# Performance work log

Measured on AMD Instinct MI355X. Metric: run time of the kernel, lower is better.

The kernel has to match this reference:

```python
import jax, jax.numpy as jnp
import numpy as np

N = 100000      # nodes
E = 1600000     # edges
G = 512         # graphs in batch
C_IN = 128
H = 256
C_OUT = 10
L = 4           # num_layers
BN_EPS = 1e-5


def setup_inputs() -> dict:
    key = jax.random.key(0)
    ks = jax.random.split(key, 24)
    x = jax.random.normal(ks[0], (N, C_IN), dtype=jnp.float32)
    src = jax.random.randint(ks[1], (E,), 0, N, dtype=jnp.int32)
    dst = jax.random.randint(ks[2], (E,), 0, N, dtype=jnp.int32)
    batch = jnp.sort(jax.random.randint(ks[3], (N,), 0, G, dtype=jnp.int32))
    s_in = 1.0 / np.sqrt(C_IN)
    s_h = 1.0 / np.sqrt(H)
    # layer 0 GIN MLP (C_IN -> H -> H)
    W1_0 = jax.random.normal(ks[4], (C_IN, H), dtype=jnp.float32) * s_in
    b1_0 = jnp.zeros((H,), dtype=jnp.float32)
    W2_0 = jax.random.normal(ks[5], (H, H), dtype=jnp.float32) * s_h
    b2_0 = jnp.zeros((H,), dtype=jnp.float32)
    # layers 1..L-1 GIN MLPs (H -> H -> H), stacked
    W1_r = jax.random.normal(ks[6], (L - 1, H, H), dtype=jnp.float32) * s_h
    b1_r = jnp.zeros((L - 1, H), dtype=jnp.float32)
    W2_r = jax.random.normal(ks[7], (L - 1, H, H), dtype=jnp.float32) * s_h
    b2_r = jnp.zeros((L - 1, H), dtype=jnp.float32)
    # BatchNorm (inference / running stats) per layer
    bn_gamma = jnp.ones((L, H), dtype=jnp.float32)
    bn_beta = jnp.zeros((L, H), dtype=jnp.float32)
    bn_mean = jax.random.normal(ks[8], (L, H), dtype=jnp.float32) * 0.1
    bn_var = jax.random.uniform(ks[9], (L, H), dtype=jnp.float32, minval=0.5, maxval=1.5)
    Wc = jax.random.normal(ks[10], (H, C_OUT), dtype=jnp.float32) * s_h
    bc = jnp.zeros((C_OUT,), dtype=jnp.float32)
    return dict(x=x, src=src, dst=dst, batch=batch,
                W1_0=W1_0, b1_0=b1_0, W2_0=W2_0, b2_0=b2_0,
                W1_r=W1_r, b1_r=b1_r, W2_r=W2_r, b2_r=b2_r,
                bn_gamma=bn_gamma, bn_beta=bn_beta, bn_mean=bn_mean, bn_var=bn_var,
                Wc=Wc, bc=bc)


def _gin_layer(x, src, dst, W1, b1, W2, b2, gamma, beta, mean, var):
    # GIN aggregation (eps=0): (1+eps)*x + sum over incoming neighbors
    agg = jax.ops.segment_sum(x[src], dst, num_segments=N)  # gather-scatter over edges
    h = x + agg
    # 2-layer MLP
    h = jax.nn.relu(h @ W1 + b1) @ W2 + b2
    # BatchNorm1d (eval, running stats) + ReLU; dropout is identity in eval
    h = (h - mean) * (gamma * jax.lax.rsqrt(var + BN_EPS)) + beta
    return jax.nn.relu(h)


def reference(x, src, dst, batch, W1_0, b1_0, W2_0, b2_0,
              W1_r, b1_r, W2_r, b2_r, bn_gamma, bn_beta, bn_mean, bn_var, Wc, bc):
    h = _gin_layer(x, src, dst, W1_0, b1_0, W2_0, b2_0,
                   bn_gamma[0], bn_beta[0], bn_mean[0], bn_var[0])
    for i in range(L - 1):
        h = _gin_layer(h, src, dst, W1_r[i], b1_r[i], W2_r[i], b2_r[i],
                       bn_gamma[i + 1], bn_beta[i + 1], bn_mean[i + 1], bn_var[i + 1])
    # global_mean_pool over graphs
    sums = jax.ops.segment_sum(h, batch, num_segments=G)            # [G, H]
    cnt = jax.ops.segment_sum(jnp.ones((N,), h.dtype), batch, num_segments=G)
    pooled = sums / jnp.maximum(cnt, 1.0)[:, None]
    return pooled @ Wc + bc
```

## Files before the change

kernel.cpp:

```cpp
#include <hip/hip_runtime.h>
#include <stdint.h>

#define NN 100000
#define NE 1600000
#define NG 512
#define NB_SCAN ((NN + 1023) / 1024)
#define BSH 8
#define NBUK ((NN + 255) >> 8)
#define BCAP 5120
#define P1CH 4096
#define NP1 ((NE + P1CH - 1) / P1CH)

typedef __attribute__((ext_vector_type(2))) float f32x2;
typedef __attribute__((ext_vector_type(2))) unsigned short u16x2;
typedef __attribute__((ext_vector_type(4))) unsigned short u16x4;
typedef __attribute__((ext_vector_type(4))) unsigned int u32x4;
typedef __attribute__((ext_vector_type(4))) int i32x4;
typedef __attribute__((ext_vector_type(8))) short bf16x8;
typedef __attribute__((ext_vector_type(4))) float f32x4;
typedef unsigned long long u64;

__device__ __forceinline__ float bf2f(unsigned short u) {
  union { unsigned int i; float f; } v; v.i = ((unsigned int)u) << 16; return v.f;
}
__device__ __forceinline__ unsigned short f2bf(float f) {
  union { float f; unsigned int i; } v; v.f = f;
  unsigned int x = v.i;
  return (unsigned short)((x + 0x7fffu + ((x >> 16) & 1u)) >> 16);
}

__global__ __launch_bounds__(256) void p1_kernel(const int* __restrict__ src,
                                                 const int* __restrict__ dst,
                                                 int* __restrict__ bcur,
                                                 u64* __restrict__ pairs) {
  __shared__ u64 buf[P1CH];
  __shared__ int cnt[NBUK], off[NBUK], place[NBUK], gbase[NBUK];
  int tid = threadIdx.x;
  int e0 = blockIdx.x * P1CH;
  int ecnt = min(P1CH, NE - e0);
  for (int i = tid; i < NBUK; i += 256) cnt[i] = 0;
  __syncthreads();
  int ls[16], ld[16];
#pragma unroll
  for (int k = 0; k < 16; ++k) {
    int i = tid + k * 256;
    if (i < ecnt) {
      ls[k] = src[e0 + i];
      ld[k] = dst[e0 + i];
      atomicAdd(&cnt[ld[k] >> BSH], 1);
    }
  }
  __syncthreads();
  if (tid < 64) {
    int base = tid * 7;
    int loc[7];
    int s = 0;
#pragma unroll
    for (int k = 0; k < 7; ++k) {
      int idx = base + k;
      int v = (idx < NBUK) ? cnt[idx] : 0;
      loc[k] = s; s += v;
    }
    int incl = s;
    for (int o = 1; o < 64; o <<= 1) {
      int t = __shfl_up(incl, o, 64);
      if (tid >= o) incl += t;
    }
    int ex = incl - s;
#pragma unroll
    for (int k = 0; k < 7; ++k) {
      int idx = base + k;
      if (idx < NBUK) { off[idx] = ex + loc[k]; place[idx] = ex + loc[k]; }
    }
  }
  __syncthreads();
  for (int b = tid; b < NBUK; b += 256)
    if (cnt[b] > 0) gbase[b] = atomicAdd(&bcur[b], cnt[b]);
  __syncthreads();
#pragma unroll
  for (int k = 0; k < 16; ++k) {
    int i = tid + k * 256;
    if (i < ecnt) {
      int b = ld[k] >> BSH;
      int p = atomicAdd(&place[b], 1);
      buf[p] = ((u64)(unsigned)ld[k] << 32) | (unsigned)ls[k];
    }
  }
  __syncthreads();
  for (int i = tid; i < ecnt; i += 256) {
    u64 pr = buf[i];
    int b = (int)(pr >> 32) >> BSH;
    int idx = gbase[b] + (i - off[b]);
    pairs[(size_t)b * BCAP + idx] = pr;
  }
}

__global__ __launch_bounds__(256) void bcount_kernel(const u64* __restrict__ pairs,
                                                     const int* __restrict__ bcur,
                                                     int* __restrict__ ncnt) {
  int b = blockIdx.x, tid = threadIdx.x;
  __shared__ int cnt[256];
  cnt[tid] = 0;
  __syncthreads();
  int n = bcur[b];
  const u64* pp = pairs + (size_t)b * BCAP;
  for (int i = tid; i < n; i += 256) {
    int d = (int)(pp[i] >> 32);
    atomicAdd(&cnt[d & 255], 1);
  }
  __syncthreads();
  int node = (b << BSH) + tid;
  if (node < NN) ncnt[node] = cnt[tid];
}

__global__ __launch_bounds__(256) void p2_kernel(const u64* __restrict__ pairs,
                                                 const int* __restrict__ bcur,
                                                 const int* __restrict__ rowptr,
                                                 int* __restrict__ esrc) {
  int b = blockIdx.x, tid = threadIdx.x;
  __shared__ int cur[256];
  int node = (b << BSH) + tid;
  cur[tid] = (node < NN) ? rowptr[node] : 0;
  __syncthreads();
  int n = bcur[b];
  const u64* pp = pairs + (size_t)b * BCAP;
  for (int i = tid; i < n; i += 256) {
    u64 pr = pp[i];
    int s = (int)(pr & 0xffffffffu);
    int d = (int)(pr >> 32);
    int p = atomicAdd(&cur[d & 255], 1);
    esrc[p] = s;
  }
}

__global__ __launch_bounds__(256) void bsum_kernel(const int* __restrict__ counts,
                                                   int* __restrict__ bsums) {
  __shared__ int red[256];
  int b = blockIdx.x, tid = threadIdx.x;
  int s = 0;
#pragma unroll
  for (int k = 0; k < 4; ++k) {
    int i = b * 1024 + k * 256 + tid;
    if (i < NN) s += counts[i];
  }
  red[tid] = s;
  __syncthreads();
  for (int off = 128; off > 0; off >>= 1) {
    if (tid < off) red[tid] += red[tid + off];
    __syncthreads();
  }
  if (tid == 0) bsums[b] = red[0];
}

__global__ __launch_bounds__(128) void bscan_kernel(const int* __restrict__ bsums,
                                                    int* __restrict__ boff,
                                                    int* __restrict__ rowptr) {
  __shared__ int buf[128];
  int tid = threadIdx.x;
  int v = (tid < NB_SCAN) ? bsums[tid] : 0;
  buf[tid] = v;
  __syncthreads();
  int incl = v;
  for (int off = 1; off < 128; off <<= 1) {
    int add = (tid >= off) ? buf[tid - off] : 0;
    __syncthreads();
    incl += add;
    buf[tid] = incl;
    __syncthreads();
  }
  if (tid < NB_SCAN) boff[tid] = incl - v;
  if (tid == NB_SCAN - 1) rowptr[NN] = incl;
}

__global__ __launch_bounds__(256) void scan_apply_kernel(const int* __restrict__ counts,
                                                         const int* __restrict__ boff,
                                                         int* __restrict__ rowptr) {
  __shared__ int tsum[256];
  int b = blockIdx.x, tid = threadIdx.x;
  int base = b * 1024 + tid * 4;
  int c[4];
  if (base + 3 < NN) {
    i32x4 cv = *(const i32x4*)(counts + base);
    c[0] = cv[0]; c[1] = cv[1]; c[2] = cv[2]; c[3] = cv[3];
  } else {
#pragma unroll
    for (int k = 0; k < 4; ++k) c[k] = (base + k < NN) ? counts[base + k] : 0;
  }
  int s = c[0] + c[1] + c[2] + c[3];
  tsum[tid] = s;
  __syncthreads();
  int incl = s;
  for (int off = 1; off < 256; off <<= 1) {
    int add = (tid >= off) ? tsum[tid - off] : 0;
    __syncthreads();
    incl += add;
    tsum[tid] = incl;
    __syncthreads();
  }
  int ex = boff[b] + incl - s;
#pragma unroll
  for (int k = 0; k < 4; ++k) {
    int i = base + k;
    if (i < NN) rowptr[i] = ex;
    ex += c[k];
  }
}

__global__ __launch_bounds__(256) void convx_kernel(const float* __restrict__ x,
                                                    unsigned short* __restrict__ xb) {
  int t = blockIdx.x * 256 + threadIdx.x;
  int i = t * 4;
  if (i < NN * 128) {
    f32x4 v = *(const f32x4*)(x + i);
    u16x4 o;
    o[0] = f2bf(v[0]); o[1] = f2bf(v[1]); o[2] = f2bf(v[2]); o[3] = f2bf(v[3]);
    *(u16x4*)(xb + i) = o;
  }
}

__global__ __launch_bounds__(256) void wconv_kernel(const float* __restrict__ W,
                                                    unsigned short* __restrict__ Wt,
                                                    int K, int ncols) {
  int t = blockIdx.x * 256 + threadIdx.x;
  if (t < K * ncols) {
    int k = t / ncols, n = t % ncols;
    Wt[n * K + k] = f2bf(W[t]);
  }
}

__global__ __launch_bounds__(256) void bnprep_kernel(const float* __restrict__ gamma,
                                                     const float* __restrict__ beta,
                                                     const float* __restrict__ mean,
                                                     const float* __restrict__ var,
                                                     float* __restrict__ scale,
                                                     float* __restrict__ shift) {
  int t = blockIdx.x * 256 + threadIdx.x;
  if (t < 4 * 256) {
    float s = gamma[t] * rsqrtf(var[t] + 1e-5f);
    scale[t] = s;
    shift[t] = beta[t] - mean[t] * s;
  }
}

__device__ __forceinline__ void deq4(int w, float s, float& a0, float& a1, float& a2, float& a3) {
  a0 += s * (float)((w << 24) >> 24);
  a1 += s * (float)((w << 16) >> 24);
  a2 += s * (float)((w << 8) >> 24);
  a3 += s * (float)(w >> 24);
}

__global__ __launch_bounds__(256, 8) void agg256_kernel(const signed char* __restrict__ hq,
                                                        const float* __restrict__ hs,
                                                        const int* __restrict__ rowptr,
                                                        const int* __restrict__ esrc,
                                                        unsigned short* __restrict__ out) {
  int node = blockIdx.x * 4 + (threadIdx.x >> 6);
  int lane = threadIdx.x & 63;
  if (node >= NN) return;
  const int* __restrict__ hv = (const int*)hq;
  float a0 = 0.f, a1 = 0.f, a2 = 0.f, a3 = 0.f;
  deq4(hv[(size_t)node * 64 + lane], hs[node], a0, a1, a2, a3);
  int p = rowptr[node];
  const int pe = rowptr[node + 1];
  for (; p + 16 <= pe; p += 16) {
    int idx[16];
#pragma unroll
    for (int j = 0; j < 16; ++j) idx[j] = esrc[p + j];
    int w[16]; float sc[16];
#pragma unroll
    for (int j = 0; j < 16; ++j) { w[j] = hv[(size_t)idx[j] * 64 + lane]; sc[j] = hs[idx[j]]; }
#pragma unroll
    for (int j = 0; j < 16; ++j) deq4(w[j], sc[j], a0, a1, a2, a3);
  }
  for (; p + 4 <= pe; p += 4) {
    int idx[4];
#pragma unroll
    for (int j = 0; j < 4; ++j) idx[j] = esrc[p + j];
    int w[4]; float sc[4];
#pragma unroll
    for (int j = 0; j < 4; ++j) { w[j] = hv[(size_t)idx[j] * 64 + lane]; sc[j] = hs[idx[j]]; }
#pragma unroll
    for (int j = 0; j < 4; ++j) deq4(w[j], sc[j], a0, a1, a2, a3);
  }
  for (; p < pe; ++p) deq4(hv[(size_t)esrc[p] * 64 + lane], hs[esrc[p]], a0, a1, a2, a3);
  u16x4 o; o[0] = f2bf(a0); o[1] = f2bf(a1); o[2] = f2bf(a2); o[3] = f2bf(a3);
  union { u16x4 v; u64 q; } cv; cv.v = o;
  __builtin_nontemporal_store(cv.q, (u64*)out + (size_t)node * 64 + lane);
}

__global__ __launch_bounds__(256, 8) void agg128_kernel(const unsigned short* __restrict__ h,
                                                        const int* __restrict__ rowptr,
                                                        const int* __restrict__ esrc,
                                                        unsigned short* __restrict__ out) {
  int node = blockIdx.x * 4 + (threadIdx.x >> 6);
  int lane = threadIdx.x & 63;
  if (node >= NN) return;
  const u16x2* __restrict__ hv = (const u16x2*)h;
  u16x2 v = hv[(size_t)node * 64 + lane];
  float a0 = bf2f(v[0]), a1 = bf2f(v[1]);
  int p = rowptr[node];
  const int pe = rowptr[node + 1];
  for (; p + 8 <= pe; p += 8) {
    int idx[8];
#pragma unroll
    for (int j = 0; j < 8; ++j) idx[j] = esrc[p + j];
    u16x2 u[8];
#pragma unroll
    for (int j = 0; j < 8; ++j) u[j] = hv[(size_t)idx[j] * 64 + lane];
#pragma unroll
    for (int j = 0; j < 8; ++j) { a0 += bf2f(u[j][0]); a1 += bf2f(u[j][1]); }
  }
  for (; p < pe; ++p) {
    u16x2 u = hv[(size_t)esrc[p] * 64 + lane];
    a0 += bf2f(u[0]); a1 += bf2f(u[1]);
  }
  u16x2 o; o[0] = f2bf(a0); o[1] = f2bf(a1);
  ((u16x2*)out)[(size_t)node * 64 + lane] = o;
}

template <int K>
__global__ __launch_bounds__(256, 4) void mlp_kernel(
    const unsigned short* __restrict__ hin, const unsigned short* __restrict__ W1t,
    const float* __restrict__ b1, const unsigned short* __restrict__ W2t,
    const float* __restrict__ b2, const float* __restrict__ bnscale,
    const float* __restrict__ bnshift, signed char* __restrict__ hq,
    float* __restrict__ hscale, int M) {
  constexpr int AP = K + 8;
  constexpr int SP = 264;
  __shared__ unsigned short buf[64 * 264];
  __shared__ float wmax[4][64];
  __shared__ float rowinv[64];
  int tid = threadIdx.x;
  int lane = tid & 63, w = tid >> 6;
  int l16 = lane & 15, lhi = lane >> 4;
  int row0 = blockIdx.x * 64;

  constexpr int CH = 64 * K / 8;
  for (int ch = tid; ch < CH; ch += 256) {
    int r = ch / (K / 8);
    int c = (ch % (K / 8)) * 8;
    u32x4 val = {0u, 0u, 0u, 0u};
    if (row0 + r < M) val = *(const u32x4*)(hin + (size_t)(row0 + r) * K + c);
    *(u32x4*)(&buf[r * AP + c]) = val;
  }
  __syncthreads();

  f32x4 acc[4][4] = {};
#pragma unroll
  for (int ks = 0; ks < K / 32; ++ks) {
    int kk = ks * 32 + lhi * 8;
    bf16x8 a[4], b[4];
#pragma unroll
    for (int mf = 0; mf < 4; ++mf)
      a[mf] = *(const bf16x8*)(&buf[(16 * mf + l16) * AP + kk]);
#pragma unroll
    for (int nf = 0; nf < 4; ++nf)
      b[nf] = *(const bf16x8*)(W1t + (size_t)(64 * w + 16 * nf + l16) * K + kk);
#pragma unroll
    for (int mf = 0; mf < 4; ++mf)
#pragma unroll
      for (int nf = 0; nf < 4; ++nf)
        acc[mf][nf] = __builtin_amdgcn_mfma_f32_16x16x32_bf16(a[mf], b[nf], acc[mf][nf], 0, 0, 0);
  }
  __syncthreads();

#pragma unroll
  for (int nf = 0; nf < 4; ++nf) {
    int col = 64 * w + 16 * nf + l16;
    float bias = b1[col];
#pragma unroll
    for (int mf = 0; mf < 4; ++mf) {
      f32x4 v = acc[mf][nf];
#pragma unroll
      for (int j = 0; j < 4; ++j) {
        float x = v[j] + bias;
        x = fmaxf(x, 0.f);
        buf[(16 * mf + lhi * 4 + j) * SP + col] = f2bf(x);
      }
    }
  }
  __syncthreads();

  f32x4 acc2[4][4] = {};
#pragma unroll
  for (int ks = 0; ks < 8; ++ks) {
    int kk = ks * 32 + lhi * 8;
    bf16x8 a[4], b[4];
#pragma unroll
    for (int mf = 0; mf < 4; ++mf)
      a[mf] = *(const bf16x8*)(&buf[(16 * mf + l16) * SP + kk]);
#pragma unroll
    for (int nf = 0; nf < 4; ++nf)
      b[nf] = *(const bf16x8*)(W2t + (size_t)(64 * w + 16 * nf + l16) * 256 + kk);
#pragma unroll
    for (int mf = 0; mf < 4; ++mf)
#pragma unroll
      for (int nf = 0; nf < 4; ++nf)
        acc2[mf][nf] = __builtin_amdgcn_mfma_f32_16x16x32_bf16(a[mf], b[nf], acc2[mf][nf], 0, 0, 0);
  }

  float pmax[4][4];
#pragma unroll
  for (int mf = 0; mf < 4; ++mf)
#pragma unroll
    for (int j = 0; j < 4; ++j) pmax[mf][j] = 0.f;
#pragma unroll
  for (int nf = 0; nf < 4; ++nf) {
    int col = 64 * w + 16 * nf + l16;
    float bias = b2[col], sc = bnscale[col], sh = bnshift[col];
#pragma unroll
    for (int mf = 0; mf < 4; ++mf) {
#pragma unroll
      for (int j = 0; j < 4; ++j) {
        float x = acc2[mf][nf][j] + bias;
        x = x * sc + sh;
        x = fmaxf(x, 0.f);
        acc2[mf][nf][j] = x;
        pmax[mf][j] = fmaxf(pmax[mf][j], x);
      }
    }
  }
#pragma unroll
  for (int mf = 0; mf < 4; ++mf) {
#pragma unroll
    for (int j = 0; j < 4; ++j) {
      float m = pmax[mf][j];
      m = fmaxf(m, __shfl_xor(m, 1, 16));
      m = fmaxf(m, __shfl_xor(m, 2, 16));
      m = fmaxf(m, __shfl_xor(m, 4, 16));
      m = fmaxf(m, __shfl_xor(m, 8, 16));
      pmax[mf][j] = m;
    }
  }
  if (l16 == 0) {
#pragma unroll
    for (int mf = 0; mf < 4; ++mf)
#pragma unroll
      for (int j = 0; j < 4; ++j)
        wmax[w][16 * mf + lhi * 4 + j] = pmax[mf][j];
  }
  __syncthreads();
  if (tid < 64) {
    float m = fmaxf(fmaxf(wmax[0][tid], wmax[1][tid]), fmaxf(wmax[2][tid], wmax[3][tid]));
    m = fmaxf(m, 1e-20f);
    rowinv[tid] = 127.f / m;
    int r = row0 + tid;
    if (r < M) hscale[r] = m * (1.f / 127.f);
  }
  __syncthreads();
#pragma unroll
  for (int mf = 0; mf < 4; ++mf) {
#pragma unroll
    for (int j = 0; j < 4; ++j) {
      int lr = 16 * mf + lhi * 4 + j;
      int r = row0 + lr;
      if (r < M) {
        float inv = rowinv[lr];
#pragma unroll
        for (int nf = 0; nf < 4; ++nf) {
          int col = 64 * w + 16 * nf + l16;
          int q = __float2int_rn(acc2[mf][nf][j] * inv);
          hq[(size_t)r * 256 + col] = (signed char)q;
        }
      }
    }
  }
}

__global__ __launch_bounds__(256) void pool_classify_kernel(
    const signed char* __restrict__ hq, const float* __restrict__ hs,
    const int* __restrict__ batch, const float* __restrict__ Wc,
    const float* __restrict__ bc, float* __restrict__ out) {
  int g = blockIdx.x;
  int tid = threadIdx.x;
  __shared__ int bounds[2];
  if (tid < 2) {
    int target = g + tid;
    int lo = 0, hi = NN;
    while (lo < hi) {
      int mid = (lo + hi) >> 1;
      if (batch[mid] < target) lo = mid + 1; else hi = mid;
    }
    bounds[tid] = lo;
  }
  __syncthreads();
  int s = bounds[0], e = bounds[1];
  float sum = 0.f;
  for (int i = s; i < e; ++i)
    sum += hs[i] * (float)hq[(size_t)i * 256 + tid];
  int cnt = e - s;
  float p = sum / (float)(cnt > 1 ? cnt : 1);
  __shared__ float red[256];
  for (int c = 0; c < 10; ++c) {
    red[tid] = p * Wc[tid * 10 + c];
    __syncthreads();
    for (int off = 128; off > 0; off >>= 1) {
      if (tid < off) red[tid] += red[tid + off];
      __syncthreads();
    }
    if (tid == 0) out[g * 10 + c] = red[0] + bc[c];
    __syncthreads();
  }
}

extern "C" void kernel_launch(void* const* d_in, const int* in_sizes, int n_in,
                              void* d_out, int out_size, void* d_ws, size_t ws_size,
                              hipStream_t stream) {
  const float* x = (const float*)d_in[0];
  const int* src = (const int*)d_in[1];
  const int* dst = (const int*)d_in[2];
  const int* batch = (const int*)d_in[3];
  const float* W1_0 = (const float*)d_in[4];
  const float* b1_0 = (const float*)d_in[5];
  const float* W2_0 = (const float*)d_in[6];
  const float* b2_0 = (const float*)d_in[7];
  const float* W1_r = (const float*)d_in[8];
  const float* b1_r = (const float*)d_in[9];
  const float* W2_r = (const float*)d_in[10];
  const float* b2_r = (const float*)d_in[11];
  const float* bn_gamma = (const float*)d_in[12];
  const float* bn_beta = (const float*)d_in[13];
  const float* bn_mean = (const float*)d_in[14];
  const float* bn_var = (const float*)d_in[15];
  const float* Wc = (const float*)d_in[16];
  const float* bc = (const float*)d_in[17];
  float* out = (float*)d_out;

  char* base = (char*)d_ws;
  size_t off = 0;
  auto take = [&](size_t bytes) {
    size_t cur = off;
    off += (bytes + 255) & ~(size_t)255;
    return cur;
  };
  int* bcur = (int*)(base + take((size_t)NBUK * 4));
  u64* pairs = (u64*)(base + take((size_t)NBUK * BCAP * 8));
  int* ncnt = (int*)(base + take((size_t)NN * 4));
  int* rowptr = (int*)(base + take((size_t)(NN + 1) * 4));
  int* esrc = (int*)(base + take((size_t)NE * 4));
  unsigned short* xb = (unsigned short*)(base + take((size_t)NN * 128 * 2));
  signed char* hq = (signed char*)(base + take((size_t)NN * 256));
  float* hscale = (float*)(base + take((size_t)NN * 4));
  unsigned short* hin = (unsigned short*)(base + take((size_t)NN * 256 * 2));
  unsigned short* W1_0t = (unsigned short*)(base + take(256 * 128 * 2));
  unsigned short* W2_0t = (unsigned short*)(base + take(256 * 256 * 2));
  unsigned short* W1_rt = (unsigned short*)(base + take(3 * 256 * 256 * 2));
  unsigned short* W2_rt = (unsigned short*)(base + take(3 * 256 * 256 * 2));
  float* bnscale = (float*)(base + take(4 * 256 * 4));
  float* bnshift = (float*)(base + take(4 * 256 * 4));
  int* bsums = (int*)(base + take(NB_SCAN * 4));
  int* boff = (int*)(base + take(NB_SCAN * 4));
  (void)ws_size; (void)in_sizes; (void)n_in; (void)out_size;

  (void)hipMemsetAsync(bcur, 0, (size_t)NBUK * 4, stream);
  p1_kernel<<<NP1, 256, 0, stream>>>(src, dst, bcur, pairs);
  bcount_kernel<<<NBUK, 256, 0, stream>>>(pairs, bcur, ncnt);
  bsum_kernel<<<NB_SCAN, 256, 0, stream>>>(ncnt, bsums);
  bscan_kernel<<<1, 128, 0, stream>>>(bsums, boff, rowptr);
  scan_apply_kernel<<<NB_SCAN, 256, 0, stream>>>(ncnt, boff, rowptr);
  p2_kernel<<<NBUK, 256, 0, stream>>>(pairs, bcur, rowptr, esrc);

  convx_kernel<<<NN * 128 / 4 / 256, 256, 0, stream>>>(x, xb);
  wconv_kernel<<<128, 256, 0, stream>>>(W1_0, W1_0t, 128, 256);
  wconv_kernel<<<256, 256, 0, stream>>>(W2_0, W2_0t, 256, 256);
  for (int i = 0; i < 3; ++i) {
    wconv_kernel<<<256, 256, 0, stream>>>(W1_r + (size_t)i * 65536, W1_rt + (size_t)i * 65536, 256, 256);
    wconv_kernel<<<256, 256, 0, stream>>>(W2_r + (size_t)i * 65536, W2_rt + (size_t)i * 65536, 256, 256);
  }
  bnprep_kernel<<<4, 256, 0, stream>>>(bn_gamma, bn_beta, bn_mean, bn_var, bnscale, bnshift);

  const int aggGrid = (NN + 3) / 4;
  const int mlpGrid = (NN + 63) / 64;

  agg128_kernel<<<aggGrid, 256, 0, stream>>>(xb, rowptr, esrc, hin);
  mlp_kernel<128><<<mlpGrid, 256, 0, stream>>>(hin, W1_0t, b1_0, W2_0t, b2_0,
                                               bnscale, bnshift, hq, hscale, NN);
  for (int i = 0; i < 3; ++i) {
    agg256_kernel<<<aggGrid, 256, 0, stream>>>(hq, hscale, rowptr, esrc, hin);
    mlp_kernel<256><<<mlpGrid, 256, 0, stream>>>(
        hin, W1_rt + (size_t)i * 65536, b1_r + (size_t)i * 256,
        W2_rt + (size_t)i * 65536, b2_r + (size_t)i * 256,
        bnscale + (size_t)(i + 1) * 256, bnshift + (size_t)(i + 1) * 256, hq, hscale, NN);
  }

  pool_classify_kernel<<<NG, 256, 0, stream>>>(hq, hscale, batch, Wc, bc, out);
}
```

Before: 717.3 us.

## Fuse neighbor aggregation into GIN MLP kernel via shared-memory staging

Merges the per-layer aggregation kernel into the MLP kernel. Each wave aggregates 16 nodes' neighbor features directly into the shared-memory A tile, so the intermediate bf16 aggregated buffer is no longer written to and read back from global memory, and one launch per layer disappears. Ping-pong int8 buffers are added because the fused kernel reads neighbors of the previous layer while writing the new layer. The cost is lower parallelism in the gather phase: fewer blocks and waves each handle 16 nodes serially, with occupancy limited by the MLP's launch bounds. Gather latency may be harder to hide as a result.

```diff
diff --git a/kernel.cpp b/kernel.cpp
--- a/kernel.cpp
+++ b/kernel.cpp
@@ -249,83 +249,14 @@
   a3 += s * (float)(w >> 24);
 }
 
-__global__ __launch_bounds__(256, 8) void agg256_kernel(const signed char* __restrict__ hq,
-                                                        const float* __restrict__ hs,
-                                                        const int* __restrict__ rowptr,
-                                                        const int* __restrict__ esrc,
-                                                        unsigned short* __restrict__ out) {
-  int node = blockIdx.x * 4 + (threadIdx.x >> 6);
-  int lane = threadIdx.x & 63;
-  if (node >= NN) return;
-  const int* __restrict__ hv = (const int*)hq;
-  float a0 = 0.f, a1 = 0.f, a2 = 0.f, a3 = 0.f;
-  deq4(hv[(size_t)node * 64 + lane], hs[node], a0, a1, a2, a3);
-  int p = rowptr[node];
-  const int pe = rowptr[node + 1];
-  for (; p + 16 <= pe; p += 16) {
-    int idx[16];
-#pragma unroll
-    for (int j = 0; j < 16; ++j) idx[j] = esrc[p + j];
-    int w[16]; float sc[16];
-#pragma unroll
-    for (int j = 0; j < 16; ++j) { w[j] = hv[(size_t)idx[j] * 64 + lane]; sc[j] = hs[idx[j]]; }
-#pragma unroll
-    for (int j = 0; j < 16; ++j) deq4(w[j], sc[j], a0, a1, a2, a3);
-  }
-  for (; p + 4 <= pe; p += 4) {
-    int idx[4];
-#pragma unroll
-    for (int j = 0; j < 4; ++j) idx[j] = esrc[p + j];
-    int w[4]; float sc[4];
-#pragma unroll
-    for (int j = 0; j < 4; ++j) { w[j] = hv[(size_t)idx[j] * 64 + lane]; sc[j] = hs[idx[j]]; }
-#pragma unroll
-    for (int j = 0; j < 4; ++j) deq4(w[j], sc[j], a0, a1, a2, a3);
-  }
-  for (; p < pe; ++p) deq4(hv[(size_t)esrc[p] * 64 + lane], hs[esrc[p]], a0, a1, a2, a3);
-  u16x4 o; o[0] = f2bf(a0); o[1] = f2bf(a1); o[2] = f2bf(a2); o[3] = f2bf(a3);
-  union { u16x4 v; u64 q; } cv; cv.v = o;
-  __builtin_nontemporal_store(cv.q, (u64*)out + (size_t)node * 64 + lane);
-}
-
-__global__ __launch_bounds__(256, 8) void agg128_kernel(const unsigned short* __restrict__ h,
-                                                        const int* __restrict__ rowptr,
-                                                        const int* __restrict__ esrc,
-                                                        unsigned short* __restrict__ out) {
-  int node = blockIdx.x * 4 + (threadIdx.x >> 6);
-  int lane = threadIdx.x & 63;
-  if (node >= NN) return;
-  const u16x2* __restrict__ hv = (const u16x2*)h;
-  u16x2 v = hv[(size_t)node * 64 + lane];
-  float a0 = bf2f(v[0]), a1 = bf2f(v[1]);
-  int p = rowptr[node];
-  const int pe = rowptr[node + 1];
-  for (; p + 8 <= pe; p += 8) {
-    int idx[8];
-#pragma unroll
-    for (int j = 0; j < 8; ++j) idx[j] = esrc[p + j];
-    u16x2 u[8];
-#pragma unroll
-    for (int j = 0; j < 8; ++j) u[j] = hv[(size_t)idx[j] * 64 + lane];
-#pragma unroll
-    for (int j = 0; j < 8; ++j) { a0 += bf2f(u[j][0]); a1 += bf2f(u[j][1]); }
-  }
-  for (; p < pe; ++p) {
-    u16x2 u = hv[(size_t)esrc[p] * 64 + lane];
-    a0 += bf2f(u[0]); a1 += bf2f(u[1]);
-  }
-  u16x2 o; o[0] = f2bf(a0); o[1] = f2bf(a1);
-  ((u16x2*)out)[(size_t)node * 64 + lane] = o;
-}
-
-template <int K>
-__global__ __launch_bounds__(256, 4) void mlp_kernel(
-    const unsigned short* __restrict__ hin, const unsigned short* __restrict__ W1t,
-    const float* __restrict__ b1, const unsigned short* __restrict__ W2t,
-    const float* __restrict__ b2, const float* __restrict__ bnscale,
-    const float* __restrict__ bnshift, signed char* __restrict__ hq,
-    float* __restrict__ hscale, int M) {
-  constexpr int AP = K + 8;
+__global__ __launch_bounds__(256, 4) void fused256_kernel(
+    const signed char* __restrict__ hqin, const float* __restrict__ hsin,
+    const int* __restrict__ rowptr, const int* __restrict__ esrc,
+    const unsigned short* __restrict__ W1t, const float* __restrict__ b1,
+    const unsigned short* __restrict__ W2t, const float* __restrict__ b2,
+    const float* __restrict__ bnscale, const float* __restrict__ bnshift,
+    signed char* __restrict__ hqout, float* __restrict__ hsout, int M) {
+  constexpr int AP = 264;
   constexpr int SP = 264;
   __shared__ unsigned short buf[64 * 264];
   __shared__ float wmax[4][64];
@@ -335,19 +266,44 @@
   int l16 = lane & 15, lhi = lane >> 4;
   int row0 = blockIdx.x * 64;
 
-  constexpr int CH = 64 * K / 8;
-  for (int ch = tid; ch < CH; ch += 256) {
-    int r = ch / (K / 8);
-    int c = (ch % (K / 8)) * 8;
-    u32x4 val = {0u, 0u, 0u, 0u};
-    if (row0 + r < M) val = *(const u32x4*)(hin + (size_t)(row0 + r) * K + c);
-    *(u32x4*)(&buf[r * AP + c]) = val;
+  const int* __restrict__ hv = (const int*)hqin;
+  for (int i = 0; i < 16; ++i) {
+    int node = row0 + (w << 4) + i;
+    float a0 = 0.f, a1 = 0.f, a2 = 0.f, a3 = 0.f;
+    if (node < M) {
+      deq4(hv[(size_t)node * 64 + lane], hsin[node], a0, a1, a2, a3);
+      int p = rowptr[node];
+      const int pe = rowptr[node + 1];
+      for (; p + 16 <= pe; p += 16) {
+        int idx[16];
+#pragma unroll
+        for (int j = 0; j < 16; ++j) idx[j] = esrc[p + j];
+        int wv[16]; float sc[16];
+#pragma unroll
+        for (int j = 0; j < 16; ++j) { wv[j] = hv[(size_t)idx[j] * 64 + lane]; sc[j] = hsin[idx[j]]; }
+#pragma unroll
+        for (int j = 0; j < 16; ++j) deq4(wv[j], sc[j], a0, a1, a2, a3);
+      }
+      for (; p + 4 <= pe; p += 4) {
+        int idx[4];
+#pragma unroll
+        for (int j = 0; j < 4; ++j) idx[j] = esrc[p + j];
+        int wv[4]; float sc[4];
+#pragma unroll
+        for (int j = 0; j < 4; ++j) { wv[j] = hv[(size_t)idx[j] * 64 + lane]; sc[j] = hsin[idx[j]]; }
+#pragma unroll
+        for (int j = 0; j < 4; ++j) deq4(wv[j], sc[j], a0, a1, a2, a3);
+      }
+      for (; p < pe; ++p) deq4(hv[(size_t)esrc[p] * 64 + lane], hsin[esrc[p]], a0, a1, a2, a3);
+    }
+    u16x4 o; o[0] = f2bf(a0); o[1] = f2bf(a1); o[2] = f2bf(a2); o[3] = f2bf(a3);
+    *(u16x4*)(&buf[((w << 4) + i) * AP + lane * 4]) = o;
   }
   __syncthreads();
 
   f32x4 acc[4][4] = {};
 #pragma unroll
-  for (int ks = 0; ks < K / 32; ++ks) {
+  for (int ks = 0; ks < 8; ++ks) {
     int kk = ks * 32 + lhi * 8;
     bf16x8 a[4], b[4];
 #pragma unroll
@@ -355,7 +311,7 @@
       a[mf] = *(const bf16x8*)(&buf[(16 * mf + l16) * AP + kk]);
 #pragma unroll
     for (int nf = 0; nf < 4; ++nf)
-      b[nf] = *(const bf16x8*)(W1t + (size_t)(64 * w + 16 * nf + l16) * K + kk);
+      b[nf] = *(const bf16x8*)(W1t + (size_t)(64 * w + 16 * nf + l16) * 256 + kk);
 #pragma unroll
     for (int mf = 0; mf < 4; ++mf)
 #pragma unroll
@@ -445,7 +401,7 @@
     m = fmaxf(m, 1e-20f);
     rowinv[tid] = 127.f / m;
     int r = row0 + tid;
-    if (r < M) hscale[r] = m * (1.f / 127.f);
+    if (r < M) hsout[r] = m * (1.f / 127.f);
   }
   __syncthreads();
 #pragma unroll
@@ -460,7 +416,175 @@
         for (int nf = 0; nf < 4; ++nf) {
           int col = 64 * w + 16 * nf + l16;
           int q = __float2int_rn(acc2[mf][nf][j] * inv);
-          hq[(size_t)r * 256 + col] = (signed char)q;
+          hqout[(size_t)r * 256 + col] = (signed char)q;
+        }
+      }
+    }
+  }
+}
+
+__global__ __launch_bounds__(256, 4) void fused128_kernel(
+    const unsigned short* __restrict__ xb,
+    const int* __restrict__ rowptr, const int* __restrict__ esrc,
+    const unsigned short* __restrict__ W1t, const float* __restrict__ b1,
+    const unsigned short* __restrict__ W2t, const float* __restrict__ b2,
+    const float* __restrict__ bnscale, const float* __restrict__ bnshift,
+    signed char* __restrict__ hqout, float* __restrict__ hsout, int M) {
+  constexpr int AP = 136;
+  constexpr int SP = 264;
+  __shared__ unsigned short buf[64 * 264];
+  __shared__ float wmax[4][64];
+  __shared__ float rowinv[64];
+  int tid = threadIdx.x;
+  int lane = tid & 63, w = tid >> 6;
+  int l16 = lane & 15, lhi = lane >> 4;
+  int row0 = blockIdx.x * 64;
+
+  const u16x2* __restrict__ hv = (const u16x2*)xb;
+  for (int i = 0; i < 16; ++i) {
+    int node = row0 + (w << 4) + i;
+    float a0 = 0.f, a1 = 0.f;
+    if (node < M) {
+      u16x2 v = hv[(size_t)node * 64 + lane];
+      a0 = bf2f(v[0]); a1 = bf2f(v[1]);
+      int p = rowptr[node];
+      const int pe = rowptr[node + 1];
+      for (; p + 8 <= pe; p += 8) {
+        int idx[8];
+#pragma unroll
+        for (int j = 0; j < 8; ++j) idx[j] = esrc[p + j];
+        u16x2 u[8];
+#pragma unroll
+        for (int j = 0; j < 8; ++j) u[j] = hv[(size_t)idx[j] * 64 + lane];
+#pragma unroll
+        for (int j = 0; j < 8; ++j) { a0 += bf2f(u[j][0]); a1 += bf2f(u[j][1]); }
+      }
+      for (; p < pe; ++p) {
+        u16x2 u = hv[(size_t)esrc[p] * 64 + lane];
+        a0 += bf2f(u[0]); a1 += bf2f(u[1]);
+      }
+    }
+    u16x2 o; o[0] = f2bf(a0); o[1] = f2bf(a1);
+    *(u16x2*)(&buf[((w << 4) + i) * AP + lane * 2]) = o;
+  }
+  __syncthreads();
+
+  f32x4 acc[4][4] = {};
+#pragma unroll
+  for (int ks = 0; ks < 4; ++ks) {
+    int kk = ks * 32 + lhi * 8;
+    bf16x8 a[4], b[4];
+#pragma unroll
+    for (int mf = 0; mf < 4; ++mf)
+      a[mf] = *(const bf16x8*)(&buf[(16 * mf + l16) * AP + kk]);
+#pragma unroll
+    for (int nf = 0; nf < 4; ++nf)
+      b[nf] = *(const bf16x8*)(W1t + (size_t)(64 * w + 16 * nf + l16) * 128 + kk);
+#pragma unroll
+    for (int mf = 0; mf < 4; ++mf)
+#pragma unroll
+      for (int nf = 0; nf < 4; ++nf)
+        acc[mf][nf] = __builtin_amdgcn_mfma_f32_16x16x32_bf16(a[mf], b[nf], acc[mf][nf], 0, 0, 0);
+  }
+  __syncthreads();
+
+#pragma unroll
+  for (int nf = 0; nf < 4; ++nf) {
+    int col = 64 * w + 16 * nf + l16;
+    float bias = b1[col];
+#pragma unroll
+    for (int mf = 0; mf < 4; ++mf) {
+      f32x4 v = acc[mf][nf];
+#pragma unroll
+      for (int j = 0; j < 4; ++j) {
+        float x = v[j] + bias;
+        x = fmaxf(x, 0.f);
+        buf[(16 * mf + lhi * 4 + j) * SP + col] = f2bf(x);
+      }
+    }
+  }
+  __syncthreads();
+
+  f32x4 acc2[4][4] = {};
+#pragma unroll
+  for (int ks = 0; ks < 8; ++ks) {
+    int kk = ks * 32 + lhi * 8;
+    bf16x8 a[4], b[4];
+#pragma unroll
+    for (int mf = 0; mf < 4; ++mf)
+      a[mf] = *(const bf16x8*)(&buf[(16 * mf + l16) * SP + kk]);
+#pragma unroll
+    for (int nf = 0; nf < 4; ++nf)
+      b[nf] = *(const bf16x8*)(W2t + (size_t)(64 * w + 16 * nf + l16) * 256 + kk);
+#pragma unroll
+    for (int mf = 0; mf < 4; ++mf)
+#pragma unroll
+      for (int nf = 0; nf < 4; ++nf)
+        acc2[mf][nf] = __builtin_amdgcn_mfma_f32_16x16x32_bf16(a[mf], b[nf], acc2[mf][nf], 0, 0, 0);
+  }
+
+  float pmax[4][4];
+#pragma unroll
+  for (int mf = 0; mf < 4; ++mf)
+#pragma unroll
+    for (int j = 0; j < 4; ++j) pmax[mf][j] = 0.f;
+#pragma unroll
+  for (int nf = 0; nf < 4; ++nf) {
+    int col = 64 * w + 16 * nf + l16;
+    float bias = b2[col], sc = bnscale[col], sh = bnshift[col];
+#pragma unroll
+    for (int mf = 0; mf < 4; ++mf) {
+#pragma unroll
+      for (int j = 0; j < 4; ++j) {
+        float x = acc2[mf][nf][j] + bias;
+        x = x * sc + sh;
+        x = fmaxf(x, 0.f);
+        acc2[mf][nf][j] = x;
+        pmax[mf][j] = fmaxf(pmax[mf][j], x);
+      }
+    }
+  }
+#pragma unroll
+  for (int mf = 0; mf < 4; ++mf) {
+#pragma unroll
+    for (int j = 0; j < 4; ++j) {
+      float m = pmax[mf][j];
+      m = fmaxf(m, __shfl_xor(m, 1, 16));
+      m = fmaxf(m, __shfl_xor(m, 2, 16));
+      m = fmaxf(m, __shfl_xor(m, 4, 16));
+      m = fmaxf(m, __shfl_xor(m, 8, 16));
+      pmax[mf][j] = m;
+    }
+  }
+  if (l16 == 0) {
+#pragma unroll
+    for (int mf = 0; mf < 4; ++mf)
+#pragma unroll
+      for (int j = 0; j < 4; ++j)
+        wmax[w][16 * mf + lhi * 4 + j] = pmax[mf][j];
+  }
+  __syncthreads();
+  if (tid < 64) {
+    float m = fmaxf(fmaxf(wmax[0][tid], wmax[1][tid]), fmaxf(wmax[2][tid], wmax[3][tid]));
+    m = fmaxf(m, 1e-20f);
+    rowinv[tid] = 127.f / m;
+    int r = row0 + tid;
+    if (r < M) hsout[r] = m * (1.f / 127.f);
+  }
+  __syncthreads();
+#pragma unroll
+  for (int mf = 0; mf < 4; ++mf) {
+#pragma unroll
+    for (int j = 0; j < 4; ++j) {
+      int lr = 16 * mf + lhi * 4 + j;
+      int r = row0 + lr;
+      if (r < M) {
+        float inv = rowinv[lr];
+#pragma unroll
+        for (int nf = 0; nf < 4; ++nf) {
+          int col = 64 * w + 16 * nf + l16;
+          int q = __float2int_rn(acc2[mf][nf][j] * inv);
+          hqout[(size_t)r * 256 + col] = (signed char)q;
         }
       }
     }
@@ -539,9 +663,10 @@
   int* rowptr = (int*)(base + take((size_t)(NN + 1) * 4));
   int* esrc = (int*)(base + take((size_t)NE * 4));
   unsigned short* xb = (unsigned short*)(base + take((size_t)NN * 128 * 2));
-  signed char* hq = (signed char*)(base + take((size_t)NN * 256));
-  float* hscale = (float*)(base + take((size_t)NN * 4));
-  unsigned short* hin = (unsigned short*)(base + take((size_t)NN * 256 * 2));
+  signed char* hqA = (signed char*)(base + take((size_t)NN * 256));
+  float* hsA = (float*)(base + take((size_t)NN * 4));
+  signed char* hqB = (signed char*)(base + take((size_t)NN * 256));
+  float* hsB = (float*)(base + take((size_t)NN * 4));
   unsigned short* W1_0t = (unsigned short*)(base + take(256 * 128 * 2));
   unsigned short* W2_0t = (unsigned short*)(base + take(256 * 256 * 2));
   unsigned short* W1_rt = (unsigned short*)(base + take(3 * 256 * 256 * 2));
@@ -569,19 +694,22 @@
   }
   bnprep_kernel<<<4, 256, 0, stream>>>(bn_gamma, bn_beta, bn_mean, bn_var, bnscale, bnshift);
 
-  const int aggGrid = (NN + 3) / 4;
-  const int mlpGrid = (NN + 63) / 64;
-
-  agg128_kernel<<<aggGrid, 256, 0, stream>>>(xb, rowptr, esrc, hin);
-  mlp_kernel<128><<<mlpGrid, 256, 0, stream>>>(hin, W1_0t, b1_0, W2_0t, b2_0,
-                                               bnscale, bnshift, hq, hscale, NN);
+  const int fusedGrid = (NN + 63) / 64;
+
+  fused128_kernel<<<fusedGrid, 256, 0, stream>>>(xb, rowptr, esrc, W1_0t, b1_0,
+                                                 W2_0t, b2_0, bnscale, bnshift,
+                                                 hqA, hsA, NN);
+  signed char* qin = hqA; float* sin_ = hsA;
+  signed char* qout = hqB; float* sout = hsB;
   for (int i = 0; i < 3; ++i) {
-    agg256_kernel<<<aggGrid, 256, 0, stream>>>(hq, hscale, rowptr, esrc, hin);
-    mlp_kernel<256><<<mlpGrid, 256, 0, stream>>>(
-        hin, W1_rt + (size_t)i * 65536, b1_r + (size_t)i * 256,
+    fused256_kernel<<<fusedGrid, 256, 0, stream>>>(
+        qin, sin_, rowptr, esrc, W1_rt + (size_t)i * 65536, b1_r + (size_t)i * 256,
         W2_rt + (size_t)i * 65536, b2_r + (size_t)i * 256,
-        bnscale + (size_t)(i + 1) * 256, bnshift + (size_t)(i + 1) * 256, hq, hscale, NN);
-  }
-
-  pool_classify_kernel<<<NG, 256, 0, stream>>>(hq, hscale, batch, Wc, bc, out);
-}
+        bnscale + (size_t)(i + 1) * 256, bnshift + (size_t)(i + 1) * 256,
+        qout, sout, NN);
+    signed char* tq = qin; qin = qout; qout = tq;
+    float* ts = sin_; sin_ = sout; sout = ts;
+  }
+
+  pool_classify_kernel<<<NG, 256, 0, stream>>>(qin, sin_, batch, Wc, bc, out);
+}
```

Result: slower. 825.3 us (+15.1%).

## Quantize aggregated features to int8 and stage MLP output stores through LDS

Applied to the files above, without the earlier changes.

The 256-wide aggregation kernel now quantizes its per-node sums to int8 with a per-row scale, found by a wavefront max-reduction, instead of writing bf16. The MLP kernel dequantizes that int8 input to bf16 while filling LDS. This halves the bytes moved between aggregation and MLP but adds another quantization step, which costs accuracy. The MLP epilogue also stages its int8 outputs in shared memory and writes them as coalesced 16-byte rows, replacing scattered single-byte global stores.

```diff
diff --git a/kernel.cpp b/kernel.cpp
--- a/kernel.cpp
+++ b/kernel.cpp
@@ -253,7 +253,8 @@
                                                         const float* __restrict__ hs,
                                                         const int* __restrict__ rowptr,
                                                         const int* __restrict__ esrc,
-                                                        unsigned short* __restrict__ out) {
+                                                        signed char* __restrict__ outq,
+                                                        float* __restrict__ outs) {
   int node = blockIdx.x * 4 + (threadIdx.x >> 6);
   int lane = threadIdx.x & 63;
   if (node >= NN) return;
@@ -283,9 +284,15 @@
     for (int j = 0; j < 4; ++j) deq4(w[j], sc[j], a0, a1, a2, a3);
   }
   for (; p < pe; ++p) deq4(hv[(size_t)esrc[p] * 64 + lane], hs[esrc[p]], a0, a1, a2, a3);
-  u16x4 o; o[0] = f2bf(a0); o[1] = f2bf(a1); o[2] = f2bf(a2); o[3] = f2bf(a3);
-  union { u16x4 v; u64 q; } cv; cv.v = o;
-  __builtin_nontemporal_store(cv.q, (u64*)out + (size_t)node * 64 + lane);
+  float m = fmaxf(fmaxf(fabsf(a0), fabsf(a1)), fmaxf(fabsf(a2), fabsf(a3)));
+  for (int o = 1; o < 64; o <<= 1) m = fmaxf(m, __shfl_xor(m, o, 64));
+  m = fmaxf(m, 1e-20f);
+  float inv = 127.f / m;
+  int q0 = __float2int_rn(a0 * inv), q1 = __float2int_rn(a1 * inv);
+  int q2 = __float2int_rn(a2 * inv), q3 = __float2int_rn(a3 * inv);
+  unsigned int pk = (q0 & 255) | ((q1 & 255) << 8) | ((q2 & 255) << 16) | ((q3 & 255) << 24);
+  ((unsigned int*)outq)[(size_t)node * 64 + lane] = pk;
+  if (lane == 0) outs[node] = m * (1.f / 127.f);
 }
 
 __global__ __launch_bounds__(256, 8) void agg128_kernel(const unsigned short* __restrict__ h,
@@ -320,7 +327,8 @@
 
 template <int K>
 __global__ __launch_bounds__(256, 4) void mlp_kernel(
-    const unsigned short* __restrict__ hin, const unsigned short* __restrict__ W1t,
+    const unsigned short* __restrict__ hinb, const signed char* __restrict__ hinq,
+    const float* __restrict__ hins, const unsigned short* __restrict__ W1t,
     const float* __restrict__ b1, const unsigned short* __restrict__ W2t,
     const float* __restrict__ b2, const float* __restrict__ bnscale,
     const float* __restrict__ bnshift, signed char* __restrict__ hq,
@@ -335,13 +343,39 @@
   int l16 = lane & 15, lhi = lane >> 4;
   int row0 = blockIdx.x * 64;
 
-  constexpr int CH = 64 * K / 8;
-  for (int ch = tid; ch < CH; ch += 256) {
-    int r = ch / (K / 8);
-    int c = (ch % (K / 8)) * 8;
-    u32x4 val = {0u, 0u, 0u, 0u};
-    if (row0 + r < M) val = *(const u32x4*)(hin + (size_t)(row0 + r) * K + c);
-    *(u32x4*)(&buf[r * AP + c]) = val;
+  if constexpr (K == 128) {
+    constexpr int CH = 64 * K / 8;
+    for (int ch = tid; ch < CH; ch += 256) {
+      int r = ch / (K / 8);
+      int c = (ch % (K / 8)) * 8;
+      u32x4 val = {0u, 0u, 0u, 0u};
+      if (row0 + r < M) val = *(const u32x4*)(hinb + (size_t)(row0 + r) * K + c);
+      *(u32x4*)(&buf[r * AP + c]) = val;
+    }
+  } else {
+    for (int ch = tid; ch < 2048; ch += 256) {
+      int r = ch >> 5;
+      int c = (ch & 31) * 8;
+      int gr = row0 + r;
+      unsigned int w0 = 0u, w1 = 0u; float s = 0.f;
+      if (gr < M) {
+        const unsigned int* p = (const unsigned int*)(hinq + (size_t)gr * 256 + c);
+        w0 = p[0]; w1 = p[1];
+        s = hins[gr];
+      }
+      u32x4 outv;
+#pragma unroll
+      for (int h = 0; h < 2; ++h) {
+        unsigned int wv = h ? w1 : w0;
+        unsigned short c0 = f2bf(s * (float)((int)(wv << 24) >> 24));
+        unsigned short c1 = f2bf(s * (float)((int)(wv << 16) >> 24));
+        unsigned short c2 = f2bf(s * (float)((int)(wv << 8) >> 24));
+        unsigned short c3 = f2bf(s * (float)((int)wv >> 24));
+        outv[2 * h] = (unsigned)c0 | ((unsigned)c1 << 16);
+        outv[2 * h + 1] = (unsigned)c2 | ((unsigned)c3 << 16);
+      }
+      *(u32x4*)(&buf[r * AP + c]) = outv;
+    }
   }
   __syncthreads();
 
@@ -448,22 +482,28 @@
     if (r < M) hscale[r] = m * (1.f / 127.f);
   }
   __syncthreads();
+
+  char* bufc = (char*)buf;
 #pragma unroll
   for (int mf = 0; mf < 4; ++mf) {
 #pragma unroll
     for (int j = 0; j < 4; ++j) {
       int lr = 16 * mf + lhi * 4 + j;
-      int r = row0 + lr;
-      if (r < M) {
-        float inv = rowinv[lr];
-#pragma unroll
-        for (int nf = 0; nf < 4; ++nf) {
-          int col = 64 * w + 16 * nf + l16;
-          int q = __float2int_rn(acc2[mf][nf][j] * inv);
-          hq[(size_t)r * 256 + col] = (signed char)q;
-        }
+      float inv = rowinv[lr];
+#pragma unroll
+      for (int nf = 0; nf < 4; ++nf) {
+        int col = 64 * w + 16 * nf + l16;
+        int q = __float2int_rn(acc2[mf][nf][j] * inv);
+        bufc[lr * 256 + col] = (char)q;
       }
     }
+  }
+  __syncthreads();
+  for (int ch = tid; ch < 64 * 16; ch += 256) {
+    int r = ch >> 4;
+    int c = (ch & 15) * 16;
+    if (row0 + r < M)
+      *(u32x4*)(hq + (size_t)(row0 + r) * 256 + c) = *(const u32x4*)(bufc + r * 256 + c);
   }
 }
 
@@ -541,6 +581,8 @@
   unsigned short* xb = (unsigned short*)(base + take((size_t)NN * 128 * 2));
   signed char* hq = (signed char*)(base + take((size_t)NN * 256));
   float* hscale = (float*)(base + take((size_t)NN * 4));
+  signed char* hinq = (signed char*)(base + take((size_t)NN * 256));
+  float* hinscale = (float*)(base + take((size_t)NN * 4));
   unsigned short* hin = (unsigned short*)(base + take((size_t)NN * 256 * 2));
   unsigned short* W1_0t = (unsigned short*)(base + take(256 * 128 * 2));
   unsigned short* W2_0t = (unsigned short*)(base + take(256 * 256 * 2));
@@ -573,12 +615,13 @@
   const int mlpGrid = (NN + 63) / 64;
 
   agg128_kernel<<<aggGrid, 256, 0, stream>>>(xb, rowptr, esrc, hin);
-  mlp_kernel<128><<<mlpGrid, 256, 0, stream>>>(hin, W1_0t, b1_0, W2_0t, b2_0,
-                                               bnscale, bnshift, hq, hscale, NN);
+  mlp_kernel<128><<<mlpGrid, 256, 0, stream>>>(hin, nullptr, nullptr, W1_0t, b1_0,
+                                               W2_0t, b2_0, bnscale, bnshift,
+                                               hq, hscale, NN);
   for (int i = 0; i < 3; ++i) {
-    agg256_kernel<<<aggGrid, 256, 0, stream>>>(hq, hscale, rowptr, esrc, hin);
+    agg256_kernel<<<aggGrid, 256, 0, stream>>>(hq, hscale, rowptr, esrc, hinq, hinscale);
     mlp_kernel<256><<<mlpGrid, 256, 0, stream>>>(
-        hin, W1_rt + (size_t)i * 65536, b1_r + (size_t)i * 256,
+        nullptr, hinq, hinscale, W1_rt + (size_t)i * 65536, b1_r + (size_t)i * 256,
         W2_rt + (size_t)i * 65536, b2_r + (size_t)i * 256,
         bnscale + (size_t)(i + 1) * 256, bnshift + (size_t)(i + 1) * 256, hq, hscale, NN);
   }
```

Measured after the change: 683.9 us. -4.7%, faster.
